# Kernel optimization log

Measured on AMD Instinct MI355X. Metric: run time of the kernel, lower is better.

## Reference

```python
import jax, jax.numpy as jnp
import numpy as np

DIM = 1024
HEADS = 16
HEAD_DIM = DIM // HEADS
SCALE = HEAD_DIM ** -0.5


def setup_inputs() -> dict:
    key = jax.random.key(0)
    ks = jax.random.split(key, 6)
    B, N, C = 2, 2048, DIM
    q = jax.random.normal(ks[0], (B, N, C), dtype=jnp.float32)
    k = jax.random.normal(ks[1], (B, N, C), dtype=jnp.float32)
    v = jax.random.normal(ks[2], (B, N, C), dtype=jnp.float32)
    # torch nn.Linear weights: out = x @ W.T (+ b); qkv has no bias (qkv_bias=False)
    W_qkv = jax.random.normal(ks[3], (3 * C, 3 * C), dtype=jnp.float32) * (3 * C) ** -0.5
    W_proj = jax.random.normal(ks[4], (C, C), dtype=jnp.float32) * C ** -0.5
    b_proj = jax.random.normal(ks[5], (C,), dtype=jnp.float32) * 0.02
    return {"q": q, "k": k, "v": v, "W_qkv": W_qkv, "W_proj": W_proj, "b_proj": b_proj}


def reference(q, k, v, W_qkv, W_proj, b_proj):
    B, N, C = q.shape
    # fused QKV projection on concatenated [q,k,v] -> [B,N,3C]
    qkv = jnp.concatenate([q, k, v], axis=-1) @ W_qkv.T
    qkv = qkv.reshape(B, N, 3, HEADS, HEAD_DIM).transpose(2, 0, 3, 1, 4)  # [3,B,H,N,hd]
    qh, kh, vh = qkv[0], qkv[1], qkv[2]
    attn = jnp.einsum('bhqd,bhkd->bhqk', qh, kh) * SCALE
    attn = jax.nn.softmax(attn, axis=-1)  # attn_drop is identity (p=0)
    x = jnp.einsum('bhqk,bhkd->bhqd', attn, vh)  # [B,H,N,hd]
    x = x.transpose(0, 2, 1, 3).reshape(B, N, C)
    x = x @ W_proj.T + b_proj  # proj_drop is identity (p=0)
    return x
```

## Files before the change

kernel.cpp:

```cpp
#include <hip/hip_runtime.h>
#include <hip/hip_bf16.h>
#include <stdint.h>

#define HEADS 16
#define HD 64
#define SEQ 2048
#define BATCH 2
#define CDIM 1024
#define MROWS (BATCH*SEQ)
#define K3C (3*CDIM)
#define ATT_SCALE 0.125f

typedef __bf16 bf16x8 __attribute__((ext_vector_type(8)));
typedef float  f32x4  __attribute__((ext_vector_type(4)));

__device__ __forceinline__ unsigned short f2bf(float f) {
    __hip_bfloat16 h = __float2bfloat16(f);
    return __builtin_bit_cast(unsigned short, h);
}
__device__ __forceinline__ unsigned int pack2bf(float a, float b) {
    return (unsigned int)f2bf(a) | ((unsigned int)f2bf(b) << 16);
}
__device__ __forceinline__ bf16x8 frag(uint4 u) { return __builtin_bit_cast(bf16x8, u); }

__device__ __forceinline__ void async16(const unsigned short* g, unsigned short* lds) {
    __builtin_amdgcn_global_load_lds(
        (const __attribute__((address_space(1))) unsigned int*)g,
        (__attribute__((address_space(3))) unsigned int*)lds, 16, 0, 0);
}


__global__ void cast_pack_A(const float* __restrict__ q, const float* __restrict__ k,
                            const float* __restrict__ v, unsigned short* __restrict__ A)
{
    const int m = blockIdx.x;
    const int t = threadIdx.x;
    const float* srcs[3] = {q, k, v};
    #pragma unroll
    for (int i = 0; i < 3; ++i) {
        float4 f = *(const float4*)(srcs[i] + (size_t)m*CDIM + t*4);
        ushort4 s;
        s.x = f2bf(f.x); s.y = f2bf(f.y); s.z = f2bf(f.z); s.w = f2bf(f.w);
        *(ushort4*)(A + (size_t)m*K3C + i*CDIM + t*4) = s;
    }
}

__global__ void cast_w(const float* __restrict__ src, unsigned short* __restrict__ dst, int n4)
{
    int idx = blockIdx.x * blockDim.x + threadIdx.x;
    if (idx < n4) {
        float4 f = ((const float4*)src)[idx];
        ushort4 s;
        s.x = f2bf(f.x); s.y = f2bf(f.y); s.z = f2bf(f.z); s.w = f2bf(f.w);
        ((ushort4*)dst)[idx] = s;
    }
}

template<int EPI>
__global__ __launch_bounds__(256, 2)
void gemm_bt(const unsigned short* __restrict__ A, const unsigned short* __restrict__ B,
             int M, int N, int K,
             unsigned short* __restrict__ qh, unsigned short* __restrict__ kh,
             unsigned short* __restrict__ vt,
             const float* __restrict__ bias, float* __restrict__ out)
{
    __shared__ __attribute__((aligned(16))) unsigned short As[128*32];
    __shared__ __attribute__((aligned(16))) unsigned short Bs[128*32];
    const int tid  = threadIdx.x;
    const int wave = tid >> 6;
    const int lane = tid & 63;
    const int l15  = lane & 15;
    const int quad = lane >> 4;
    const int wm = (wave >> 1) * 64;
    const int wn = (wave & 1) * 64;
    const int m0 = blockIdx.x * 128;
    const int n0 = blockIdx.y * 128;

    f32x4 acc[4][4] = {};

    const int srow = tid >> 2;
    const int sc8  = (tid & 3) * 8;

    for (int k0 = 0; k0 < K; k0 += 32) {
        #pragma unroll
        for (int t = 0; t < 2; ++t) {
            int row = t*64 + srow;
            const unsigned short* ga = A + (size_t)(m0 + row)*K + k0 + sc8;
            const unsigned short* gb = B + (size_t)(n0 + row)*K + k0 + sc8;
            async16(ga, &As[(t*256 + wave*64)*8]);
            async16(gb, &Bs[(t*256 + wave*64)*8]);
        }
        __syncthreads();
        uint4 af[4], bfv[4];
        #pragma unroll
        for (int i = 0; i < 4; ++i) {
            af[i]  = *(const uint4*)&As[(wm + i*16 + l15)*32 + quad*8];
            bfv[i] = *(const uint4*)&Bs[(wn + i*16 + l15)*32 + quad*8];
        }
        #pragma unroll
        for (int mi = 0; mi < 4; ++mi)
            #pragma unroll
            for (int ni = 0; ni < 4; ++ni)
                acc[mi][ni] = __builtin_amdgcn_mfma_f32_16x16x32_bf16(
                    frag(af[mi]), frag(bfv[ni]), acc[mi][ni], 0, 0, 0);
        __syncthreads();
    }

    if constexpr (EPI == 0) {
        #pragma unroll
        for (int mi = 0; mi < 4; ++mi) {
            int row0 = m0 + wm + mi*16 + quad*4;
            int b  = row0 >> 11;
            int nq = row0 & 2047;
            #pragma unroll
            for (int ni = 0; ni < 4; ++ni) {
                int col   = n0 + wn + ni*16 + l15;
                int which = col >> 10;
                int h     = (col >> 6) & 15;
                int d     = col & 63;
                int bh    = b*HEADS + h;
                if (which == 2) {
                    ushort4 pv;
                    pv.x = f2bf(acc[mi][ni][0]);
                    pv.y = f2bf(acc[mi][ni][1]);
                    pv.z = f2bf(acc[mi][ni][2]);
                    pv.w = f2bf(acc[mi][ni][3]);
                    *(ushort4*)&vt[((size_t)bh*HD + d)*SEQ + nq] = pv;
                } else {
                    unsigned short* dst = (which == 0) ? qh : kh;
                    float sc = (which == 0) ? ATT_SCALE : 1.0f;
                    #pragma unroll
                    for (int r = 0; r < 4; ++r)
                        dst[((size_t)bh*SEQ + nq + r)*HD + d] = f2bf(acc[mi][ni][r] * sc);
                }
            }
        }
    } else {
        #pragma unroll
        for (int mi = 0; mi < 4; ++mi) {
            int row0 = m0 + wm + mi*16 + quad*4;
            #pragma unroll
            for (int ni = 0; ni < 4; ++ni) {
                int col  = n0 + wn + ni*16 + l15;
                float bv = bias[col];
                #pragma unroll
                for (int r = 0; r < 4; ++r)
                    out[(size_t)(row0 + r)*N + col] = acc[mi][ni][r] + bv;
            }
        }
    }
}

__global__ __launch_bounds__(256, 2)
void attention(const unsigned short* __restrict__ qh, const unsigned short* __restrict__ kh,
               const unsigned short* __restrict__ vt, unsigned short* __restrict__ xb)
{
    const int qt = blockIdx.x;
    const int h  = blockIdx.y;
    const int b  = blockIdx.z;
    const int bh = b*HEADS + h;
    const int tid  = threadIdx.x;
    const int wave = tid >> 6;
    const int lane = tid & 63;
    const int l15  = lane & 15;
    const int quad = lane >> 4;

    __shared__ __attribute__((aligned(16))) unsigned short Ks[64*72];
    __shared__ __attribute__((aligned(16))) unsigned short Vs[64*72];
    __shared__ __attribute__((aligned(16))) unsigned short Ps[4][16*72];

    const unsigned short* Qp = qh + ((size_t)bh*SEQ + qt*64)*HD;
    const unsigned short* Kp = kh + (size_t)bh*SEQ*HD;
    const unsigned short* Vp = vt + (size_t)bh*HD*SEQ;

    uint4 qf0 = *(const uint4*)(Qp + (size_t)(wave*16 + l15)*HD + quad*8);
    uint4 qf1 = *(const uint4*)(Qp + (size_t)(wave*16 + l15)*HD + 32 + quad*8);

    f32x4 o[4] = {};
    float m_s = -INFINITY, l_s = 0.f;

    unsigned short* Pl = Ps[wave];

    for (int kt = 0; kt < SEQ/64; ++kt) {
        __syncthreads();
        #pragma unroll
        for (int t = 0; t < 2; ++t) {
            int rr = t*32 + (tid >> 3);
            int c8 = (tid & 7) * 8;
            *(uint4*)&Ks[rr*72 + c8] = *(const uint4*)(Kp + ((size_t)(kt*64 + rr))*HD + c8);
            *(uint4*)&Vs[rr*72 + c8] = *(const uint4*)(Vp + (size_t)rr*SEQ + kt*64 + c8);
        }
        __syncthreads();

        f32x4 s[4];
        #pragma unroll
        for (int st = 0; st < 4; ++st) {
            uint4 kf0 = *(const uint4*)&Ks[(st*16 + l15)*72 + quad*8];
            uint4 kf1 = *(const uint4*)&Ks[(st*16 + l15)*72 + 32 + quad*8];
            f32x4 z = {};
            z = __builtin_amdgcn_mfma_f32_16x16x32_bf16(frag(kf0), frag(qf0), z, 0, 0, 0);
            z = __builtin_amdgcn_mfma_f32_16x16x32_bf16(frag(kf1), frag(qf1), z, 0, 0, 0);
            s[st] = z;
        }

        float mloc = s[0][0];
        #pragma unroll
        for (int st = 0; st < 4; ++st)
            #pragma unroll
            for (int r = 0; r < 4; ++r)
                mloc = fmaxf(mloc, s[st][r]);
        mloc = fmaxf(mloc, __shfl_xor(mloc, 16));
        mloc = fmaxf(mloc, __shfl_xor(mloc, 32));

        float mn = fmaxf(m_s, mloc);
        float al = __expf(m_s - mn);
        m_s = mn;

        float p[4][4];
        float rs = 0.f;
        #pragma unroll
        for (int st = 0; st < 4; ++st)
            #pragma unroll
            for (int r = 0; r < 4; ++r) { p[st][r] = __expf(s[st][r] - mn); rs += p[st][r]; }
        rs += __shfl_xor(rs, 16);
        rs += __shfl_xor(rs, 32);
        l_s = al*l_s + rs;

        #pragma unroll
        for (int st = 0; st < 4; ++st)
            #pragma unroll
            for (int r = 0; r < 4; ++r)
                o[st][r] *= al;

        #pragma unroll
        for (int st = 0; st < 4; ++st) {
            uint2 pk;
            pk.x = pack2bf(p[st][0], p[st][1]);
            pk.y = pack2bf(p[st][2], p[st][3]);
            *(uint2*)&Pl[l15*72 + st*16 + quad*4] = pk;
        }
        asm volatile("s_waitcnt lgkmcnt(0)" ::: "memory");

        uint4 pB0 = *(const uint4*)&Pl[l15*72 + quad*8];
        uint4 pB1 = *(const uint4*)&Pl[l15*72 + 32 + quad*8];

        #pragma unroll
        for (int st = 0; st < 4; ++st) {
            uint4 vf0 = *(const uint4*)&Vs[(st*16 + l15)*72 + quad*8];
            uint4 vf1 = *(const uint4*)&Vs[(st*16 + l15)*72 + 32 + quad*8];
            o[st] = __builtin_amdgcn_mfma_f32_16x16x32_bf16(frag(vf0), frag(pB0), o[st], 0, 0, 0);
            o[st] = __builtin_amdgcn_mfma_f32_16x16x32_bf16(frag(vf1), frag(pB1), o[st], 0, 0, 0);
        }
    }

    float inv = 1.0f / l_s;
    #pragma unroll
    for (int st = 0; st < 4; ++st) {
        uint2 pk;
        pk.x = pack2bf(o[st][0]*inv, o[st][1]*inv);
        pk.y = pack2bf(o[st][2]*inv, o[st][3]*inv);
        *(uint2*)&Pl[l15*72 + st*16 + quad*4] = pk;
    }
    asm volatile("s_waitcnt lgkmcnt(0)" ::: "memory");

    const int qr = lane >> 2;
    const int dd = (lane & 3) * 16;
    uint4 oa = *(const uint4*)&Pl[qr*72 + dd];
    uint4 ob = *(const uint4*)&Pl[qr*72 + dd + 8];
    const int mrow = b*SEQ + qt*64 + wave*16 + qr;
    *(uint4*)&xb[(size_t)mrow*CDIM + h*HD + dd]     = oa;
    *(uint4*)&xb[(size_t)mrow*CDIM + h*HD + dd + 8] = ob;
}

extern "C" void kernel_launch(void* const* d_in, const int* in_sizes, int n_in,
                              void* d_out, int out_size, void* d_ws, size_t ws_size,
                              hipStream_t stream)
{
    const float* q  = (const float*)d_in[0];
    const float* k  = (const float*)d_in[1];
    const float* v  = (const float*)d_in[2];
    const float* Wq = (const float*)d_in[3];
    const float* Wp = (const float*)d_in[4];
    const float* bp = (const float*)d_in[5];
    float* out = (float*)d_out;

    char* p = (char*)d_ws;
    auto carve = [&](size_t bytes) { char* r = p; p += (bytes + 255) & ~(size_t)255; return r; };
    unsigned short* Abuf   = (unsigned short*)carve((size_t)MROWS*K3C*2);
    unsigned short* Wqkvb  = (unsigned short*)carve((size_t)K3C*K3C*2);
    unsigned short* Wprojb = (unsigned short*)carve((size_t)CDIM*CDIM*2);
    unsigned short* qhb    = (unsigned short*)carve((size_t)BATCH*HEADS*SEQ*HD*2);
    unsigned short* khb    = (unsigned short*)carve((size_t)BATCH*HEADS*SEQ*HD*2);
    unsigned short* vtb    = (unsigned short*)carve((size_t)BATCH*HEADS*SEQ*HD*2);
    unsigned short* xbuf   = (unsigned short*)carve((size_t)MROWS*CDIM*2);

    cast_pack_A<<<MROWS, 256, 0, stream>>>(q, k, v, Abuf);
    cast_w<<<(K3C*K3C/4 + 255)/256, 256, 0, stream>>>(Wq, Wqkvb, K3C*K3C/4);
    cast_w<<<(CDIM*CDIM/4 + 255)/256, 256, 0, stream>>>(Wp, Wprojb, CDIM*CDIM/4);

    gemm_bt<0><<<dim3(MROWS/128, K3C/128), 256, 0, stream>>>(
        Abuf, Wqkvb, MROWS, K3C, K3C, qhb, khb, vtb, nullptr, nullptr);

    attention<<<dim3(SEQ/64, HEADS, BATCH), 256, 0, stream>>>(qhb, khb, vtb, xbuf);

    gemm_bt<1><<<dim3(MROWS/128, CDIM/128), 256, 0, stream>>>(
        xbuf, Wprojb, MROWS, CDIM, CDIM, nullptr, nullptr, nullptr, bp, out);
}
```

Before: 313.4 us.

## Deepen GEMM K-tile to 64 and process 128 query rows per attention block

```diff
diff --git a/kernel.cpp b/kernel.cpp
--- a/kernel.cpp
+++ b/kernel.cpp
@@ -64,8 +64,8 @@
              unsigned short* __restrict__ vt,
              const float* __restrict__ bias, float* __restrict__ out)
 {
-    __shared__ __attribute__((aligned(16))) unsigned short As[128*32];
-    __shared__ __attribute__((aligned(16))) unsigned short Bs[128*32];
+    __shared__ __attribute__((aligned(16))) unsigned short As[2*128*32];
+    __shared__ __attribute__((aligned(16))) unsigned short Bs[2*128*32];
     const int tid  = threadIdx.x;
     const int wave = tid >> 6;
     const int lane = tid & 63;
@@ -81,28 +81,32 @@
     const int srow = tid >> 2;
     const int sc8  = (tid & 3) * 8;
 
-    for (int k0 = 0; k0 < K; k0 += 32) {
-        #pragma unroll
-        for (int t = 0; t < 2; ++t) {
-            int row = t*64 + srow;
-            const unsigned short* ga = A + (size_t)(m0 + row)*K + k0 + sc8;
-            const unsigned short* gb = B + (size_t)(n0 + row)*K + k0 + sc8;
+    for (int k0 = 0; k0 < K; k0 += 64) {
+        #pragma unroll
+        for (int t = 0; t < 4; ++t) {
+            int row  = (t & 1) * 64 + srow;
+            int col  = (t >> 1) * 32 + sc8;
+            const unsigned short* ga = A + (size_t)(m0 + row)*K + k0 + col;
+            const unsigned short* gb = B + (size_t)(n0 + row)*K + k0 + col;
             async16(ga, &As[(t*256 + wave*64)*8]);
             async16(gb, &Bs[(t*256 + wave*64)*8]);
         }
         __syncthreads();
-        uint4 af[4], bfv[4];
-        #pragma unroll
-        for (int i = 0; i < 4; ++i) {
-            af[i]  = *(const uint4*)&As[(wm + i*16 + l15)*32 + quad*8];
-            bfv[i] = *(const uint4*)&Bs[(wn + i*16 + l15)*32 + quad*8];
-        }
-        #pragma unroll
-        for (int mi = 0; mi < 4; ++mi)
-            #pragma unroll
-            for (int ni = 0; ni < 4; ++ni)
-                acc[mi][ni] = __builtin_amdgcn_mfma_f32_16x16x32_bf16(
-                    frag(af[mi]), frag(bfv[ni]), acc[mi][ni], 0, 0, 0);
+        #pragma unroll
+        for (int kk = 0; kk < 2; ++kk) {
+            uint4 af[4], bfv[4];
+            #pragma unroll
+            for (int i = 0; i < 4; ++i) {
+                af[i]  = *(const uint4*)&As[kk*4096 + (wm + i*16 + l15)*32 + quad*8];
+                bfv[i] = *(const uint4*)&Bs[kk*4096 + (wn + i*16 + l15)*32 + quad*8];
+            }
+            #pragma unroll
+            for (int mi = 0; mi < 4; ++mi)
+                #pragma unroll
+                for (int ni = 0; ni < 4; ++ni)
+                    acc[mi][ni] = __builtin_amdgcn_mfma_f32_16x16x32_bf16(
+                        frag(af[mi]), frag(bfv[ni]), acc[mi][ni], 0, 0, 0);
+        }
         __syncthreads();
     }
 
@@ -167,19 +171,24 @@
 
     __shared__ __attribute__((aligned(16))) unsigned short Ks[64*72];
     __shared__ __attribute__((aligned(16))) unsigned short Vs[64*72];
-    __shared__ __attribute__((aligned(16))) unsigned short Ps[4][16*72];
-
-    const unsigned short* Qp = qh + ((size_t)bh*SEQ + qt*64)*HD;
+    __shared__ __attribute__((aligned(16))) unsigned short Ps[4][2*16*72];
+
+    const unsigned short* Qp = qh + ((size_t)bh*SEQ + qt*128 + wave*32)*HD;
     const unsigned short* Kp = kh + (size_t)bh*SEQ*HD;
     const unsigned short* Vp = vt + (size_t)bh*HD*SEQ;
 
-    uint4 qf0 = *(const uint4*)(Qp + (size_t)(wave*16 + l15)*HD + quad*8);
-    uint4 qf1 = *(const uint4*)(Qp + (size_t)(wave*16 + l15)*HD + 32 + quad*8);
-
-    f32x4 o[4] = {};
-    float m_s = -INFINITY, l_s = 0.f;
-
-    unsigned short* Pl = Ps[wave];
+    uint4 qf[2][2];
+    #pragma unroll
+    for (int g = 0; g < 2; ++g) {
+        qf[g][0] = *(const uint4*)(Qp + (size_t)(g*16 + l15)*HD + quad*8);
+        qf[g][1] = *(const uint4*)(Qp + (size_t)(g*16 + l15)*HD + 32 + quad*8);
+    }
+
+    f32x4 o[2][4] = {};
+    float m_s[2] = {-INFINITY, -INFINITY};
+    float l_s[2] = {0.f, 0.f};
+
+    unsigned short* Pw = Ps[wave];
 
     for (int kt = 0; kt < SEQ/64; ++kt) {
         __syncthreads();
@@ -192,84 +201,103 @@
         }
         __syncthreads();
 
-        f32x4 s[4];
+        f32x4 s[2][4];
         #pragma unroll
         for (int st = 0; st < 4; ++st) {
             uint4 kf0 = *(const uint4*)&Ks[(st*16 + l15)*72 + quad*8];
             uint4 kf1 = *(const uint4*)&Ks[(st*16 + l15)*72 + 32 + quad*8];
-            f32x4 z = {};
-            z = __builtin_amdgcn_mfma_f32_16x16x32_bf16(frag(kf0), frag(qf0), z, 0, 0, 0);
-            z = __builtin_amdgcn_mfma_f32_16x16x32_bf16(frag(kf1), frag(qf1), z, 0, 0, 0);
-            s[st] = z;
-        }
-
-        float mloc = s[0][0];
-        #pragma unroll
-        for (int st = 0; st < 4; ++st)
-            #pragma unroll
-            for (int r = 0; r < 4; ++r)
-                mloc = fmaxf(mloc, s[st][r]);
-        mloc = fmaxf(mloc, __shfl_xor(mloc, 16));
-        mloc = fmaxf(mloc, __shfl_xor(mloc, 32));
-
-        float mn = fmaxf(m_s, mloc);
-        float al = __expf(m_s - mn);
-        m_s = mn;
-
-        float p[4][4];
-        float rs = 0.f;
-        #pragma unroll
-        for (int st = 0; st < 4; ++st)
-            #pragma unroll
-            for (int r = 0; r < 4; ++r) { p[st][r] = __expf(s[st][r] - mn); rs += p[st][r]; }
-        rs += __shfl_xor(rs, 16);
-        rs += __shfl_xor(rs, 32);
-        l_s = al*l_s + rs;
-
-        #pragma unroll
-        for (int st = 0; st < 4; ++st)
-            #pragma unroll
-            for (int r = 0; r < 4; ++r)
-                o[st][r] *= al;
-
-        #pragma unroll
-        for (int st = 0; st < 4; ++st) {
-            uint2 pk;
-            pk.x = pack2bf(p[st][0], p[st][1]);
-            pk.y = pack2bf(p[st][2], p[st][3]);
-            *(uint2*)&Pl[l15*72 + st*16 + quad*4] = pk;
+            #pragma unroll
+            for (int g = 0; g < 2; ++g) {
+                f32x4 z = {};
+                z = __builtin_amdgcn_mfma_f32_16x16x32_bf16(frag(kf0), frag(qf[g][0]), z, 0, 0, 0);
+                z = __builtin_amdgcn_mfma_f32_16x16x32_bf16(frag(kf1), frag(qf[g][1]), z, 0, 0, 0);
+                s[g][st] = z;
+            }
+        }
+
+        #pragma unroll
+        for (int g = 0; g < 2; ++g) {
+            float mloc = s[g][0][0];
+            #pragma unroll
+            for (int st = 0; st < 4; ++st)
+                #pragma unroll
+                for (int r = 0; r < 4; ++r)
+                    mloc = fmaxf(mloc, s[g][st][r]);
+            mloc = fmaxf(mloc, __shfl_xor(mloc, 16));
+            mloc = fmaxf(mloc, __shfl_xor(mloc, 32));
+
+            float mn = fmaxf(m_s[g], mloc);
+            float al = __expf(m_s[g] - mn);
+            m_s[g] = mn;
+
+            float rs = 0.f;
+            float p[4][4];
+            #pragma unroll
+            for (int st = 0; st < 4; ++st)
+                #pragma unroll
+                for (int r = 0; r < 4; ++r) { p[st][r] = __expf(s[g][st][r] - mn); rs += p[st][r]; }
+            rs += __shfl_xor(rs, 16);
+            rs += __shfl_xor(rs, 32);
+            l_s[g] = al*l_s[g] + rs;
+
+            #pragma unroll
+            for (int st = 0; st < 4; ++st)
+                #pragma unroll
+                for (int r = 0; r < 4; ++r)
+                    o[g][st][r] *= al;
+
+            #pragma unroll
+            for (int st = 0; st < 4; ++st) {
+                uint2 pk;
+                pk.x = pack2bf(p[st][0], p[st][1]);
+                pk.y = pack2bf(p[st][2], p[st][3]);
+                *(uint2*)&Pw[g*1152 + l15*72 + st*16 + quad*4] = pk;
+            }
         }
         asm volatile("s_waitcnt lgkmcnt(0)" ::: "memory");
 
-        uint4 pB0 = *(const uint4*)&Pl[l15*72 + quad*8];
-        uint4 pB1 = *(const uint4*)&Pl[l15*72 + 32 + quad*8];
+        uint4 pB[2][2];
+        #pragma unroll
+        for (int g = 0; g < 2; ++g) {
+            pB[g][0] = *(const uint4*)&Pw[g*1152 + l15*72 + quad*8];
+            pB[g][1] = *(const uint4*)&Pw[g*1152 + l15*72 + 32 + quad*8];
+        }
 
         #pragma unroll
         for (int st = 0; st < 4; ++st) {
             uint4 vf0 = *(const uint4*)&Vs[(st*16 + l15)*72 + quad*8];
             uint4 vf1 = *(const uint4*)&Vs[(st*16 + l15)*72 + 32 + quad*8];
-            o[st] = __builtin_amdgcn_mfma_f32_16x16x32_bf16(frag(vf0), frag(pB0), o[st], 0, 0, 0);
-            o[st] = __builtin_amdgcn_mfma_f32_16x16x32_bf16(frag(vf1), frag(pB1), o[st], 0, 0, 0);
-        }
-    }
-
-    float inv = 1.0f / l_s;
+            #pragma unroll
+            for (int g = 0; g < 2; ++g) {
+                o[g][st] = __builtin_amdgcn_mfma_f32_16x16x32_bf16(frag(vf0), frag(pB[g][0]), o[g][st], 0, 0, 0);
+                o[g][st] = __builtin_amdgcn_mfma_f32_16x16x32_bf16(frag(vf1), frag(pB[g][1]), o[g][st], 0, 0, 0);
+            }
+        }
+    }
+
     #pragma unroll
-    for (int st = 0; st < 4; ++st) {
-        uint2 pk;
-        pk.x = pack2bf(o[st][0]*inv, o[st][1]*inv);
-        pk.y = pack2bf(o[st][2]*inv, o[st][3]*inv);
-        *(uint2*)&Pl[l15*72 + st*16 + quad*4] = pk;
+    for (int g = 0; g < 2; ++g) {
+        float inv = 1.0f / l_s[g];
+        #pragma unroll
+        for (int st = 0; st < 4; ++st) {
+            uint2 pk;
+            pk.x = pack2bf(o[g][st][0]*inv, o[g][st][1]*inv);
+            pk.y = pack2bf(o[g][st][2]*inv, o[g][st][3]*inv);
+            *(uint2*)&Pw[g*1152 + l15*72 + st*16 + quad*4] = pk;
+        }
     }
     asm volatile("s_waitcnt lgkmcnt(0)" ::: "memory");
 
     const int qr = lane >> 2;
     const int dd = (lane & 3) * 16;
-    uint4 oa = *(const uint4*)&Pl[qr*72 + dd];
-    uint4 ob = *(const uint4*)&Pl[qr*72 + dd + 8];
-    const int mrow = b*SEQ + qt*64 + wave*16 + qr;
-    *(uint4*)&xb[(size_t)mrow*CDIM + h*HD + dd]     = oa;
-    *(uint4*)&xb[(size_t)mrow*CDIM + h*HD + dd + 8] = ob;
+    #pragma unroll
+    for (int g = 0; g < 2; ++g) {
+        uint4 oa = *(const uint4*)&Pw[g*1152 + qr*72 + dd];
+        uint4 ob = *(const uint4*)&Pw[g*1152 + qr*72 + dd + 8];
+        const int mrow = b*SEQ + qt*128 + wave*32 + g*16 + qr;
+        *(uint4*)&xb[(size_t)mrow*CDIM + h*HD + dd]     = oa;
+        *(uint4*)&xb[(size_t)mrow*CDIM + h*HD + dd + 8] = ob;
+    }
 }
 
 extern "C" void kernel_launch(void* const* d_in, const int* in_sizes, int n_in,
@@ -301,7 +329,7 @@
     gemm_bt<0><<<dim3(MROWS/128, K3C/128), 256, 0, stream>>>(
         Abuf, Wqkvb, MROWS, K3C, K3C, qhb, khb, vtb, nullptr, nullptr);
 
-    attention<<<dim3(SEQ/64, HEADS, BATCH), 256, 0, stream>>>(qhb, khb, vtb, xbuf);
+    attention<<<dim3(SEQ/128, HEADS, BATCH), 256, 0, stream>>>(qhb, khb, vtb, xbuf);
 
     gemm_bt<1><<<dim3(MROWS/128, CDIM/128), 256, 0, stream>>>(
         xbuf, Wprojb, MROWS, CDIM, CDIM, nullptr, nullptr, nullptr, bp, out);
```

New measurement: 324.8 us. 1.04x slower.

## Double-buffer attention K/V with async LDS loads, XOR swizzle, fuse cast kernels

Applied to the files above, without the earlier changes.

```diff
diff --git a/kernel.cpp b/kernel.cpp
--- a/kernel.cpp
+++ b/kernel.cpp
@@ -29,30 +29,35 @@
         (__attribute__((address_space(3))) unsigned int*)lds, 16, 0, 0);
 }
 
-
-__global__ void cast_pack_A(const float* __restrict__ q, const float* __restrict__ k,
-                            const float* __restrict__ v, unsigned short* __restrict__ A)
+__global__ void cast_all(const float* __restrict__ q, const float* __restrict__ k,
+                         const float* __restrict__ v, const float* __restrict__ Wq,
+                         const float* __restrict__ Wp,
+                         unsigned short* __restrict__ A, unsigned short* __restrict__ Wqb,
+                         unsigned short* __restrict__ Wpb)
 {
-    const int m = blockIdx.x;
+    const int bid = blockIdx.x;
     const int t = threadIdx.x;
-    const float* srcs[3] = {q, k, v};
-    #pragma unroll
-    for (int i = 0; i < 3; ++i) {
-        float4 f = *(const float4*)(srcs[i] + (size_t)m*CDIM + t*4);
+    if (bid < MROWS) {
+        const float* srcs[3] = {q, k, v};
+        #pragma unroll
+        for (int i = 0; i < 3; ++i) {
+            float4 f = *(const float4*)(srcs[i] + (size_t)bid*CDIM + t*4);
+            ushort4 s;
+            s.x = f2bf(f.x); s.y = f2bf(f.y); s.z = f2bf(f.z); s.w = f2bf(f.w);
+            *(ushort4*)(A + (size_t)bid*K3C + i*CDIM + t*4) = s;
+        }
+    } else if (bid < MROWS + 9216) {
+        int idx = (bid - MROWS)*256 + t;
+        float4 f = ((const float4*)Wq)[idx];
         ushort4 s;
         s.x = f2bf(f.x); s.y = f2bf(f.y); s.z = f2bf(f.z); s.w = f2bf(f.w);
-        *(ushort4*)(A + (size_t)m*K3C + i*CDIM + t*4) = s;
-    }
-}
-
-__global__ void cast_w(const float* __restrict__ src, unsigned short* __restrict__ dst, int n4)
-{
-    int idx = blockIdx.x * blockDim.x + threadIdx.x;
-    if (idx < n4) {
-        float4 f = ((const float4*)src)[idx];
+        ((ushort4*)Wqb)[idx] = s;
+    } else {
+        int idx = (bid - MROWS - 9216)*256 + t;
+        float4 f = ((const float4*)Wp)[idx];
         ushort4 s;
         s.x = f2bf(f.x); s.y = f2bf(f.y); s.z = f2bf(f.z); s.w = f2bf(f.w);
-        ((ushort4*)dst)[idx] = s;
+        ((ushort4*)Wpb)[idx] = s;
     }
 }
 
@@ -165,14 +170,27 @@
     const int l15  = lane & 15;
     const int quad = lane >> 4;
 
-    __shared__ __attribute__((aligned(16))) unsigned short Ks[64*72];
-    __shared__ __attribute__((aligned(16))) unsigned short Vs[64*72];
+    __shared__ __attribute__((aligned(16))) unsigned short Ks[2][64*64];
+    __shared__ __attribute__((aligned(16))) unsigned short Vs[2][64*64];
     __shared__ __attribute__((aligned(16))) unsigned short Ps[4][16*72];
 
     const unsigned short* Qp = qh + ((size_t)bh*SEQ + qt*64)*HD;
     const unsigned short* Kp = kh + (size_t)bh*SEQ*HD;
     const unsigned short* Vp = vt + (size_t)bh*HD*SEQ;
 
+    auto stage = [&](int kt, int bufI) {
+        #pragma unroll
+        for (int t = 0; t < 2; ++t) {
+            int c  = t*256 + wave*64 + lane;
+            int r  = c >> 3;
+            int cc = (c & 7) ^ (r & 7);
+            async16(Kp + (size_t)(kt*64 + r)*HD + cc*8,
+                    &Ks[bufI][(t*256 + wave*64)*8]);
+            async16(Vp + (size_t)r*SEQ + kt*64 + cc*8,
+                    &Vs[bufI][(t*256 + wave*64)*8]);
+        }
+    };
+
     uint4 qf0 = *(const uint4*)(Qp + (size_t)(wave*16 + l15)*HD + quad*8);
     uint4 qf1 = *(const uint4*)(Qp + (size_t)(wave*16 + l15)*HD + 32 + quad*8);
 
@@ -180,23 +198,24 @@
     float m_s = -INFINITY, l_s = 0.f;
 
     unsigned short* Pl = Ps[wave];
+    const int x7 = l15 & 7;
+
+    stage(0, 0);
 
     for (int kt = 0; kt < SEQ/64; ++kt) {
-        __syncthreads();
-        #pragma unroll
-        for (int t = 0; t < 2; ++t) {
-            int rr = t*32 + (tid >> 3);
-            int c8 = (tid & 7) * 8;
-            *(uint4*)&Ks[rr*72 + c8] = *(const uint4*)(Kp + ((size_t)(kt*64 + rr))*HD + c8);
-            *(uint4*)&Vs[rr*72 + c8] = *(const uint4*)(Vp + (size_t)rr*SEQ + kt*64 + c8);
-        }
-        __syncthreads();
+        stage((kt + 1) & 31, (kt + 1) & 1);
+        asm volatile("s_waitcnt vmcnt(4)" ::: "memory");
+        asm volatile("s_barrier" ::: "memory");
+
+        const unsigned short* Kb = Ks[kt & 1];
+        const unsigned short* Vb = Vs[kt & 1];
 
         f32x4 s[4];
         #pragma unroll
         for (int st = 0; st < 4; ++st) {
-            uint4 kf0 = *(const uint4*)&Ks[(st*16 + l15)*72 + quad*8];
-            uint4 kf1 = *(const uint4*)&Ks[(st*16 + l15)*72 + 32 + quad*8];
+            int rb = st*16 + l15;
+            uint4 kf0 = *(const uint4*)&Kb[(rb*8 + (quad ^ x7))*8];
+            uint4 kf1 = *(const uint4*)&Kb[(rb*8 + ((4 + quad) ^ x7))*8];
             f32x4 z = {};
             z = __builtin_amdgcn_mfma_f32_16x16x32_bf16(frag(kf0), frag(qf0), z, 0, 0, 0);
             z = __builtin_amdgcn_mfma_f32_16x16x32_bf16(frag(kf1), frag(qf1), z, 0, 0, 0);
@@ -246,11 +265,14 @@
 
         #pragma unroll
         for (int st = 0; st < 4; ++st) {
-            uint4 vf0 = *(const uint4*)&Vs[(st*16 + l15)*72 + quad*8];
-            uint4 vf1 = *(const uint4*)&Vs[(st*16 + l15)*72 + 32 + quad*8];
+            int rb = st*16 + l15;
+            uint4 vf0 = *(const uint4*)&Vb[(rb*8 + (quad ^ x7))*8];
+            uint4 vf1 = *(const uint4*)&Vb[(rb*8 + ((4 + quad) ^ x7))*8];
             o[st] = __builtin_amdgcn_mfma_f32_16x16x32_bf16(frag(vf0), frag(pB0), o[st], 0, 0, 0);
             o[st] = __builtin_amdgcn_mfma_f32_16x16x32_bf16(frag(vf1), frag(pB1), o[st], 0, 0, 0);
         }
+
+        asm volatile("s_barrier" ::: "memory");
     }
 
     float inv = 1.0f / l_s;
@@ -262,6 +284,7 @@
         *(uint2*)&Pl[l15*72 + st*16 + quad*4] = pk;
     }
     asm volatile("s_waitcnt lgkmcnt(0)" ::: "memory");
+    __syncthreads();
 
     const int qr = lane >> 2;
     const int dd = (lane & 3) * 16;
@@ -294,9 +317,7 @@
     unsigned short* vtb    = (unsigned short*)carve((size_t)BATCH*HEADS*SEQ*HD*2);
     unsigned short* xbuf   = (unsigned short*)carve((size_t)MROWS*CDIM*2);
 
-    cast_pack_A<<<MROWS, 256, 0, stream>>>(q, k, v, Abuf);
-    cast_w<<<(K3C*K3C/4 + 255)/256, 256, 0, stream>>>(Wq, Wqkvb, K3C*K3C/4);
-    cast_w<<<(CDIM*CDIM/4 + 255)/256, 256, 0, stream>>>(Wp, Wprojb, CDIM*CDIM/4);
+    cast_all<<<MROWS + 9216 + 1024, 256, 0, stream>>>(q, k, v, Wq, Wp, Abuf, Wqkvb, Wprojb);
 
     gemm_bt<0><<<dim3(MROWS/128, K3C/128), 256, 0, stream>>>(
         Abuf, Wqkvb, MROWS, K3C, K3C, qhb, khb, vtb, nullptr, nullptr);
```

After: 314.5 us. About the same (+0.3%).
